# Kernel optimization log

Hardware: AMD Instinct MI355X
Metric: run time of the kernel (lower is better)

Reference implementation:

```python
import jax, jax.numpy as jnp
import numpy as np

# ---- dims ----
B0, CIN, Hh, Ww = 8, 256, 96, 96
SPLIT = 8
DM = CIN // SPLIT            # 32  per-split d_model
EXPAND = 2
DIN = EXPAND * DM            # 64  d_inner
DSTATE = 64
DCONV = 3
HEADDIM = 8
NH = DIN // HEADDIM          # 8 heads
DOUT = 256
CHUNK = 32
D_IN_PROJ = 2 * DIN + 2 * DSTATE + NH  # 264
CONV_CH = DIN + 2 * DSTATE   # 192


def setup_inputs() -> dict:
    key = jax.random.key(0)
    ks = jax.random.split(key, 10)
    x = jax.random.normal(ks[0], (B0, CIN, Hh, Ww), jnp.float32)
    inp = {
        'x': x,
        'ln_w': jnp.ones((CIN,), jnp.float32),
        'ln_b': jnp.zeros((CIN,), jnp.float32),
        'skip_scale': jnp.ones((1,), jnp.float32),
        'proj_w': jax.random.normal(ks[1], (CIN, DOUT), jnp.float32) / np.sqrt(CIN),
        'proj_b': jnp.zeros((DOUT,), jnp.float32),
        'W_in': jax.random.normal(ks[2], (DM, D_IN_PROJ), jnp.float32) / np.sqrt(DM),
        'conv_w': jax.random.normal(ks[3], (CONV_CH, 1, DCONV), jnp.float32) * 0.3,
        'conv_b': jnp.zeros((CONV_CH,), jnp.float32),
        'dt_bias': jax.random.normal(ks[4], (NH,), jnp.float32) * 0.5,
        'A_log': jnp.log(jnp.arange(1.0, NH + 1.0, dtype=jnp.float32)),
        'D': jax.random.normal(ks[5], (NH,), jnp.float32) * 0.5,
        'rms_w': jnp.ones((DIN,), jnp.float32),
        'W_out': jax.random.normal(ks[6], (DIN, DM), jnp.float32) / np.sqrt(DIN),
    }
    return inp


def _layernorm(x, w, b, eps=1e-5):
    mu = jnp.mean(x, -1, keepdims=True)
    xc = x - mu
    var = jnp.mean(xc * xc, -1, keepdims=True)
    return xc * jax.lax.rsqrt(var + eps) * w + b


def _ssd(x, A, Bm, Cm, chunk):
    # x: (b,l,h,p)  A: (b,l,h)  Bm/Cm: (b,l,n); chunked SSD (Mamba2 minimal)
    b, l, h, p = x.shape
    n = Bm.shape[-1]
    nc = l // chunk
    xc = x.reshape(b, nc, chunk, h, p)
    Ac = A.reshape(b, nc, chunk, h).transpose(0, 3, 1, 2)  # (b,h,c,l)
    Bc = Bm.reshape(b, nc, chunk, n)
    Cc = Cm.reshape(b, nc, chunk, n)
    ac = jnp.cumsum(Ac, -1)                                 # (b,h,c,l)
    seg = ac[..., :, None] - ac[..., None, :]
    mask = jnp.tril(jnp.ones((chunk, chunk), bool))
    L = jnp.where(mask, jnp.exp(jnp.where(mask, seg, 0.0)), 0.0)  # (b,h,c,l,s)
    Yd = jnp.einsum('bcln,bcsn,bhcls,bcshp->bclhp', Cc, Bc, L, xc)
    decay_states = jnp.exp(ac[..., -1:] - ac)               # (b,h,c,l)
    states = jnp.einsum('bcln,bhcl,bclhp->bchpn', Bc, decay_states, xc)
    chunk_decay = jnp.exp(ac[..., -1])                      # (b,h,c)
    def step(carry, inp):
        s, d = inp
        return carry * d[..., None, None] + s, carry
    states_t = jnp.moveaxis(states, 1, 0)                   # (c,b,h,p,n)
    dec_t = jnp.moveaxis(chunk_decay, 2, 0)                 # (c,b,h)
    _, prev = jax.lax.scan(step, jnp.zeros_like(states_t[0]), (states_t, dec_t))
    prev = jnp.moveaxis(prev, 0, 1)                         # (b,c,h,p,n)
    Yo = jnp.einsum('bcln,bchpn,bhcl->bclhp', Cc, prev, jnp.exp(ac))
    return (Yd + Yo).reshape(b, l, h, p)


def _mamba2(u, W_in, conv_w, conv_b, dt_bias, A_log, D, rms_w, W_out):
    b, l, _ = u.shape
    zxbcdt = u @ W_in
    z = zxbcdt[..., :DIN]
    xBC = zxbcdt[..., DIN:DIN + CONV_CH]
    dt = jax.nn.softplus(zxbcdt[..., -NH:] + dt_bias)       # (b,l,h)
    conv = jax.lax.conv_general_dilated(
        xBC.transpose(0, 2, 1), conv_w, (1,), [(DCONV - 1, 0)],
        dimension_numbers=('NCH', 'OIH', 'NCH'), feature_group_count=CONV_CH)
    xBC = jax.nn.silu(conv + conv_b[None, :, None]).transpose(0, 2, 1)
    xs = xBC[..., :DIN].reshape(b, l, NH, HEADDIM)
    Bm = xBC[..., DIN:DIN + DSTATE]
    Cm = xBC[..., DIN + DSTATE:]
    A = -jnp.exp(A_log)
    y = _ssd(xs * dt[..., None], dt * A, Bm, Cm, CHUNK)
    y = y + xs * D[None, None, :, None]
    y = y.reshape(b, l, DIN) * jax.nn.silu(z)               # gated
    y = y * jax.lax.rsqrt(jnp.mean(y * y, -1, keepdims=True) + 1e-5) * rms_w
    return y @ W_out


def reference(x, ln_w, ln_b, skip_scale, proj_w, proj_b, W_in, conv_w, conv_b,
              dt_bias, A_log, D, rms_w, W_out):
    Bn, C, h, w = x.shape
    L = h * w
    xf = x.reshape(Bn, C, L).transpose(0, 2, 1)             # (B,L,C)
    xn = _layernorm(xf, ln_w, ln_b)
    d = C // SPLIT
    xs = jnp.moveaxis(xn.reshape(Bn, L, SPLIT, d), 2, 0)    # (S,B,L,d)
    xs = xs.reshape(SPLIT * Bn, L, d)
    ym = _mamba2(xs, W_in, conv_w, conv_b, dt_bias, A_log, D, rms_w, W_out)
    ym = ym + skip_scale * xs
    ym = jnp.moveaxis(ym.reshape(SPLIT, Bn, L, d), 0, 2).reshape(Bn, L, C)
    ym = _layernorm(ym, ln_w, ln_b)
    out = ym @ proj_w + proj_b                              # (B,L,DOUT)
    return out.transpose(0, 2, 1).reshape(Bn, DOUT, h, w)
```

## Files before the change

### kernel.cpp

```cpp
#include <hip/hip_runtime.h>
#include <hip/hip_fp16.h>
#include <math.h>

typedef unsigned short u16;
typedef unsigned int u32;
typedef _Float16 half2_t __attribute__((ext_vector_type(2)));
typedef _Float16 f16x8 __attribute__((ext_vector_type(8)));
typedef float f32x4 __attribute__((ext_vector_type(4)));

#define B0N 8
#define LSEQ 9216
#define NSEQ 64
#define NCHUNK 288
#define DM 32
#define DPROJ 264
#define CONVCH 192
#define XC4 208
#define URH 40
#define CHH 204
#define ZBS 66
#define CH2S 129
#define TTS 40
#define GS 36

#ifndef __has_builtin
#define __has_builtin(x) 0
#endif

__device__ __forceinline__ float silu_(float v) { return v / (1.f + __expf(-v)); }

__global__ __launch_bounds__(256) void k1_ln_split(const float* __restrict__ x,
                                                   const float* __restrict__ lnw,
                                                   const float* __restrict__ lnb,
                                                   __half* __restrict__ u) {
  __shared__ float tile[256 * 33];
  __shared__ float mu[32], rs[32], wv[256], bv[256];
  const int b = blockIdx.y, l0 = blockIdx.x * 32, t = threadIdx.x;
  wv[t] = lnw[t];
  bv[t] = lnb[t];
#pragma unroll 4
  for (int i = 0; i < 32; ++i) {
    int c = i * 8 + (t >> 5), ll = t & 31;
    tile[c * 33 + ll] = x[((size_t)b * 256 + c) * LSEQ + l0 + ll];
  }
  __syncthreads();
  if (t < 32) {
    float s = 0.f, s2 = 0.f;
    for (int c = 0; c < 256; ++c) {
      float v = tile[c * 33 + t];
      s += v; s2 += v * v;
    }
    float m = s * (1.f / 256.f);
    mu[t] = m;
    rs[t] = rsqrtf(s2 * (1.f / 256.f) - m * m + 1e-5f);
  }
  __syncthreads();
#pragma unroll 4
  for (int i = 0; i < 32; ++i) {
    int sp = i >> 2, sub = i & 3;
    int ll = sub * 8 + (t >> 5), dm = t & 31;
    int c = sp * 32 + dm;
    float v = (tile[c * 33 + ll] - mu[ll]) * rs[ll] * wv[c] + bv[c];
    u[(((size_t)(sp * B0N + b)) * LSEQ + l0 + ll) * DM + dm] = __float2half(v);
  }
}

__global__ __launch_bounds__(256, 2) void k2_states(
    const __half* __restrict__ u, const float* __restrict__ Win,
    const float* __restrict__ convw, const float* __restrict__ convb,
    const float* __restrict__ dtbias, const float* __restrict__ Alog,
    __half* __restrict__ S, float* __restrict__ cdec) {
  __shared__ __align__(16) _Float16 ur_h[48 * URH];
  __shared__ __align__(16) float CH2[34 * CH2S];
  __shared__ __align__(16) _Float16 xst[64 * TTS];
  __shared__ __align__(16) _Float16 Bt[64 * TTS];
  __shared__ __align__(16) float dtraw[256], dtv[256], acs[256], wv2[256];
  const int c = blockIdx.x, sq = blockIdx.y, t = threadIdx.x;
  const int l0 = c * 32;
  const int lane = t & 63, wvi = t >> 6, g = lane >> 4, c16 = lane & 15;
  const size_t ubase = (size_t)sq * (LSEQ * DM);
  const f32x4 zero4 = {0.f, 0.f, 0.f, 0.f};

  for (int idx = t; idx < 48 * 32; idx += 256) {
    int r = idx >> 5, dm = idx & 31;
    int l = l0 - 2 + r;
    _Float16 v = (_Float16)0.f;
    if (r < 34 && l >= 0) v = ((const _Float16*)u)[ubase + (size_t)l * DM + dm];
    ur_h[r * URH + dm] = v;
  }
  f16x8 bfr[2];
#pragma unroll
  for (int i = 0; i < 2; ++i) {
    int col = 64 + (wvi + i * 4) * 16 + c16;
#pragma unroll
    for (int j = 0; j < 8; ++j) bfr[i][j] = (_Float16)Win[(g * 8 + j) * DPROJ + col];
  }
  __syncthreads();

  {
    f16x8 am[3];
#pragma unroll
    for (int mt = 0; mt < 3; ++mt)
      am[mt] = *(const f16x8*)&ur_h[(mt * 16 + c16) * URH + g * 8];
#pragma unroll
    for (int i = 0; i < 2; ++i) {
      int colc = (wvi + i * 4) * 16 + c16;
#pragma unroll
      for (int mt = 0; mt < 3; ++mt) {
        f32x4 acc = __builtin_amdgcn_mfma_f32_16x16x32_f16(am[mt], bfr[i], zero4, 0, 0, 0);
#pragma unroll
        for (int r = 0; r < 4; ++r) {
          int R = mt * 16 + 4 * g + r;
          if (R < 34) CH2[R * CH2S + colc] = acc[r];
        }
      }
    }
  }
  __syncthreads();

  {
    const int ch0 = t & 63, lb = t >> 6;
    float cw[2][3], cb[2];
#pragma unroll
    for (int cr = 0; cr < 2; ++cr) {
      int ch = ch0 + cr * 64;
      cw[cr][0] = convw[ch * 3 + 0];
      cw[cr][1] = convw[ch * 3 + 1];
      cw[cr][2] = convw[ch * 3 + 2];
      cb[cr] = convb[ch];
    }
#pragma unroll
    for (int lr = 0; lr < 8; ++lr) {
      int l = lb + lr * 4;
#pragma unroll
      for (int cr = 0; cr < 2; ++cr) {
        int ch = ch0 + cr * 64;
        float v = CH2[l * CH2S + ch] * cw[cr][0] + CH2[(l + 1) * CH2S + ch] * cw[cr][1] +
                  CH2[(l + 2) * CH2S + ch] * cw[cr][2] + cb[cr];
        _Float16 sv = (_Float16)silu_(v);
        if (cr == 0) xst[ch * TTS + l] = sv;
        else Bt[(ch - 64) * TTS + l] = sv;
      }
    }
    int l = t >> 3, h = t & 7;
    float raw = 0.f;
#pragma unroll
    for (int dm = 0; dm < 32; ++dm)
      raw += (float)ur_h[(l + 2) * URH + dm] * Win[dm * DPROJ + 256 + h];
    dtraw[l * 8 + h] = raw;
  }
  __syncthreads();

  {
    const int l = t & 31, h = t >> 5;
    float raw = dtraw[l * 8 + h] + dtbias[h];
    float dt = (raw > 20.f) ? raw : log1pf(__expf(raw));
    float x = dt;
#pragma unroll
    for (int d = 1; d < 32; d <<= 1) {
      float y = __shfl_up(x, d, 32);
      if (l >= d) x += y;
    }
    const float A = -__expf(Alog[h]);
    dtv[t] = dt;
    acs[t] = A * x;
    if (l == 31) cdec[(sq * NCHUNK + c) * 8 + h] = __expf(A * x);
  }
  __syncthreads();

  _Float16* Ah = (_Float16*)CH2;
  {
    int h = t >> 5;
    wv2[t] = __expf(acs[h * 32 + 31] - acs[t]) * dtv[t];
  }
  __syncthreads();
  {
    const int hp = t >> 2, lb2 = (t & 3) * 8;
    const float* w = &wv2[(hp >> 3) * 32 + lb2];
    const _Float16* xr = &xst[hp * TTS + lb2];
    _Float16* ar = &Ah[hp * TTS + lb2];
#pragma unroll
    for (int i = 0; i < 8; ++i) ar[i] = (_Float16)((float)xr[i] * w[i]);
  }
  __syncthreads();

  __half* Sout = (__half*)((char*)CH2 + 5120);
  {
    const int mt = wvi;
    f16x8 aS = *(const f16x8*)&Ah[(mt * 16 + c16) * TTS + g * 8];
#pragma unroll
    for (int nt = 0; nt < 4; ++nt) {
      f16x8 bS = *(const f16x8*)&Bt[(nt * 16 + c16) * TTS + g * 8];
      f32x4 acc = __builtin_amdgcn_mfma_f32_16x16x32_f16(aS, bS, zero4, 0, 0, 0);
#pragma unroll
      for (int r = 0; r < 4; ++r)
        Sout[(mt * 16 + 4 * g + r) * 72 + nt * 16 + c16] = __float2half(acc[r]);
    }
  }
  __syncthreads();
  const size_t sbase = (size_t)(sq * NCHUNK + c) * 4096;
#pragma unroll
  for (int i = 0; i < 2; ++i) {
    int idx = i * 256 + t;
    int hp = idx >> 3, part = idx & 7;
    *(uint4*)(S + sbase + hp * 64 + part * 8) = *(const uint4*)&Sout[hp * 72 + part * 8];
  }
}

__global__ __launch_bounds__(512) void k3_scan(__half* __restrict__ S,
                                               const float* __restrict__ cdec) {
  const int sq = blockIdx.x >> 3, h = blockIdx.x & 7, t = threadIdx.x;
  float carry = 0.f;
  for (int c = 0; c < NCHUNK; ++c) {
    size_t idx = (size_t)(sq * NCHUNK + c) * 4096 + h * 512 + t;
    float s = __half2float(S[idx]);
    S[idx] = __float2half(carry);
    carry = carry * cdec[(sq * NCHUNK + c) * 8 + h] + s;
  }
}

__global__ __launch_bounds__(256, 4) void k4_out(
    const __half* __restrict__ u, const float* __restrict__ Win,
    const float* __restrict__ convw, const float* __restrict__ convb,
    const float* __restrict__ dtbias, const float* __restrict__ Alog,
    const float* __restrict__ Dp, const float* __restrict__ rmsw,
    const float* __restrict__ Wout, const float* __restrict__ skip,
    const __half* __restrict__ S, __half* __restrict__ ym) {
  __shared__ __align__(16) _Float16 ur_h[48 * URH];
  __shared__ __align__(16) _Float16 CHh[34 * CHH];
  __shared__ __align__(16) __half xch[32 * XC4];
  __shared__ __align__(16) float dtraw[256];
  __shared__ __align__(16) float dtv[256], acs[256];
  __shared__ __align__(16) _Float16 zbuf[32 * ZBS];
  const int c = blockIdx.x, sq = blockIdx.y, t = threadIdx.x;
  const int l0 = c * 32;
  const int lane = t & 63, wvi = t >> 6, g = lane >> 4, c16 = lane & 15;
  const size_t ubase = (size_t)sq * (LSEQ * DM);
  const f32x4 zero4 = {0.f, 0.f, 0.f, 0.f};

  const size_t sbase = (size_t)(sq * NCHUNK + c) * 4096;
  uint4 sv0, sv1;
  {
    const uint4* sp = (const uint4*)(S + sbase);
    sv0 = sp[t * 2];
    sv1 = sp[t * 2 + 1];
  }
  for (int idx = t; idx < 48 * 32; idx += 256) {
    int r = idx >> 5, dm = idx & 31;
    int l = l0 - 2 + r;
    _Float16 v = (_Float16)0.f;
    if (r < 34 && l >= 0) v = ((const _Float16*)u)[ubase + (size_t)l * DM + dm];
    ur_h[r * URH + dm] = v;
  }
  f16x8 bfr[3];
#pragma unroll
  for (int i = 0; i < 3; ++i) {
    int col = 64 + (wvi + i * 4) * 16 + c16;
#pragma unroll
    for (int j = 0; j < 8; ++j) bfr[i][j] = (_Float16)Win[(g * 8 + j) * DPROJ + col];
  }
  f16x8 bz;
  {
    int col = wvi * 16 + c16;
#pragma unroll
    for (int j = 0; j < 8; ++j) bz[j] = (_Float16)Win[(g * 8 + j) * DPROJ + col];
  }
  __syncthreads();

  {
    f16x8 am[3];
#pragma unroll
    for (int mt = 0; mt < 3; ++mt)
      am[mt] = *(const f16x8*)&ur_h[(mt * 16 + c16) * URH + g * 8];
#pragma unroll
    for (int i = 0; i < 3; ++i) {
      int colc = (wvi + i * 4) * 16 + c16;
#pragma unroll
      for (int mt = 0; mt < 3; ++mt) {
        f32x4 acc = __builtin_amdgcn_mfma_f32_16x16x32_f16(am[mt], bfr[i], zero4, 0, 0, 0);
#pragma unroll
        for (int r = 0; r < 4; ++r) {
          int R = mt * 16 + 4 * g + r;
          if (R < 34) CHh[R * CHH + colc] = (_Float16)acc[r];
        }
      }
    }
#pragma unroll
    for (int mz = 0; mz < 2; ++mz) {
      f16x8 az = *(const f16x8*)&ur_h[(2 + mz * 16 + c16) * URH + g * 8];
      f32x4 acc = __builtin_amdgcn_mfma_f32_16x16x32_f16(az, bz, zero4, 0, 0, 0);
#pragma unroll
      for (int r = 0; r < 4; ++r) {
        int lY = mz * 16 + 4 * g + r;
        zbuf[lY * ZBS + wvi * 16 + c16] = (_Float16)acc[r];
      }
    }
  }
  __syncthreads();

  {
    const int ch0 = t & 63, lbq = t >> 6;
#pragma unroll
    for (int cr = 0; cr < 3; ++cr) {
      int ch = ch0 + cr * 64;
      float w0 = convw[ch * 3 + 0], w1 = convw[ch * 3 + 1], w2 = convw[ch * 3 + 2];
      float cb = convb[ch];
      float a = (float)CHh[(lbq * 8 + 0) * CHH + ch];
      float b = (float)CHh[(lbq * 8 + 1) * CHH + ch];
#pragma unroll
      for (int j = 0; j < 8; ++j) {
        float cn = (float)CHh[(lbq * 8 + j + 2) * CHH + ch];
        float v = a * w0 + b * w1 + cn * w2 + cb;
        xch[(lbq * 8 + j) * XC4 + ch] = __float2half(silu_(v));
        a = b; b = cn;
      }
    }
    int l = t >> 3, h = t & 7;
    float raw = 0.f;
#pragma unroll
    for (int dm = 0; dm < 32; ++dm)
      raw += (float)ur_h[(l + 2) * URH + dm] * Win[dm * DPROJ + 256 + h];
    dtraw[l * 8 + h] = raw;
  }
  __syncthreads();

  {
    char* pvb = (char*)CHh;
    int hp = t >> 2, part = t & 3;
    *(uint4*)(pvb + hp * 144 + part * 32) = sv0;
    *(uint4*)(pvb + hp * 144 + part * 32 + 16) = sv1;
  }
  {
    const int l = t & 31, h = t >> 5;
    float raw = dtraw[l * 8 + h] + dtbias[h];
    float dt = (raw > 20.f) ? raw : log1pf(__expf(raw));
    float x = dt;
#pragma unroll
    for (int d = 1; d < 32; d <<= 1) {
      float y = __shfl_up(x, d, 32);
      if (l >= d) x += y;
    }
    dtv[t] = dt;
    acs[t] = -__expf(Alog[h]) * x;
  }
  __syncthreads();

  float* Gm = (float*)((char*)CHh + 9216);
  {
    float ev = __expf(acs[t]);
    dtraw[t] = ev;
    const int mt = wvi >> 1, nt = wvi & 1;
    f32x4 acc = zero4;
#pragma unroll
    for (int kk = 0; kk < 2; ++kk) {
      f16x8 aC = *(const f16x8*)&xch[(mt * 16 + c16) * XC4 + 128 + kk * 32 + g * 8];
      f16x8 bB = *(const f16x8*)&xch[(nt * 16 + c16) * XC4 + 64 + kk * 32 + g * 8];
      acc = __builtin_amdgcn_mfma_f32_16x16x32_f16(aC, bB, acc, 0, 0, 0);
    }
#pragma unroll
    for (int r = 0; r < 4; ++r)
      Gm[(mt * 16 + 4 * g + r) * GS + nt * 16 + c16] = acc[r];
  }
  __syncthreads();

  {
    const int s2b = g * 8;
    float gv[2][8];
#pragma unroll
    for (int mt = 0; mt < 2; ++mt) {
      const float* gr = &Gm[(mt * 16 + c16) * GS + s2b];
      float4 g0 = *(const float4*)gr;
      float4 g1 = *(const float4*)(gr + 4);
      gv[mt][0] = g0.x; gv[mt][1] = g0.y; gv[mt][2] = g0.z; gv[mt][3] = g0.w;
      gv[mt][4] = g1.x; gv[mt][5] = g1.y; gv[mt][6] = g1.z; gv[mt][7] = g1.w;
    }
#pragma unroll
    for (int hh = 0; hh < 2; ++hh) {
      const int h = 2 * wvi + hh;
      const float* ap = &acs[h * 32 + s2b];
      const float* dp = &dtv[h * 32 + s2b];
      float4 a0 = *(const float4*)ap, a1 = *(const float4*)(ap + 4);
      float4 d0 = *(const float4*)dp, d1 = *(const float4*)(dp + 4);
      const float av[8] = {a0.x, a0.y, a0.z, a0.w, a1.x, a1.y, a1.z, a1.w};
      const float dv[8] = {d0.x, d0.y, d0.z, d0.w, d1.x, d1.y, d1.z, d1.w};
      f16x8 bfr2;
#pragma unroll
      for (int j = 0; j < 8; ++j)
        bfr2[j] = *(const _Float16*)&xch[(s2b + j) * XC4 + h * 8 + (c16 & 7)];
#pragma unroll
      for (int mt = 0; mt < 2; ++mt) {
        const int row = mt * 16 + c16;
        const float arow = acs[h * 32 + row];
        f16x8 afr;
#pragma unroll
        for (int j = 0; j < 8; ++j) {
          float m = gv[mt][j] * __expf(arow - av[j]) * dv[j];
          afr[j] = (_Float16)((s2b + j <= row) ? m : 0.f);
        }
        f32x4 dacc = __builtin_amdgcn_mfma_f32_16x16x32_f16(afr, bfr2, zero4, 0, 0, 0);
        if (c16 < 8) {
#pragma unroll
          for (int r = 0; r < 4; ++r)
            xch[(mt * 16 + 4 * g + r) * XC4 + 64 + h * 8 + c16] = __float2half(dacc[r]);
        }
      }
    }
  }
  __syncthreads();

  {
    const __half* pvh = (const __half*)CHh;
#pragma unroll
    for (int mt = 0; mt < 2; ++mt) {
      f32x4 acc = zero4;
#pragma unroll
      for (int kk = 0; kk < 2; ++kk) {
        f16x8 aC = *(const f16x8*)&xch[(mt * 16 + c16) * XC4 + 128 + kk * 32 + g * 8];
        f16x8 bP = *(const f16x8*)&pvh[(wvi * 16 + c16) * 72 + kk * 32 + g * 8];
        acc = __builtin_amdgcn_mfma_f32_16x16x32_f16(aC, bP, acc, 0, 0, 0);
      }
      int hp = wvi * 16 + c16;
#pragma unroll
      for (int r = 0; r < 4; ++r) {
        int l = mt * 16 + 4 * g + r;
        float e = dtraw[(hp >> 3) * 32 + l];
        __half* yb = &xch[l * XC4 + 64 + hp];
        *yb = __float2half(__half2float(*yb) + acc[r] * e);
      }
    }
  }
  __syncthreads();

  {
    const int hp = t & 63;
    const float dcoef = Dp[hp >> 3];
#pragma unroll
    for (int k = 0; k < 8; ++k) {
      int l = (k * 256 + t) >> 6;
      float y = __half2float(xch[l * XC4 + 64 + hp]) + (float)xch[l * XC4 + hp] * dcoef;
      float z = (float)zbuf[l * ZBS + hp];
      y *= z / (1.f + __expf(-z));
      xch[l * XC4 + 64 + hp] = __float2half(y);
    }
  }
  __syncthreads();

  float* rp = Gm;
  float* scl = (float*)ur_h;
  {
    const int l = t & 31, seg = t >> 5;
    float p = 0.f;
#pragma unroll
    for (int k = 0; k < 8; ++k) {
      float v = __half2float(xch[l * XC4 + 64 + seg * 8 + k]);
      p += v * v;
    }
    rp[l * 9 + seg] = p;
  }
  __syncthreads();
  if (t < 32) {
    float s2s = 0.f;
#pragma unroll
    for (int seg = 0; seg < 8; ++seg) s2s += rp[t * 9 + seg];
    scl[t] = rsqrtf(s2s * (1.f / 64.f) + 1e-5f);
  }
  __syncthreads();

  for (int idx = t; idx < 2048; idx += 256) {
    int l = idx >> 6, hp = idx & 63;
    xch[l * XC4 + 64 + hp] =
        __float2half(__half2float(xch[l * XC4 + 64 + hp]) * scl[l] * rmsw[hp]);
  }
  __syncthreads();

  {
    const float skipv = skip[0];
    const int mt = wvi >> 1, nt = wvi & 1;
    f32x4 acc = zero4;
#pragma unroll
    for (int kk = 0; kk < 2; ++kk) {
      f16x8 aY = *(const f16x8*)&xch[(mt * 16 + c16) * XC4 + 64 + kk * 32 + g * 8];
      f16x8 bW;
#pragma unroll
      for (int j = 0; j < 8; ++j)
        bW[j] = (_Float16)Wout[(kk * 32 + g * 8 + j) * 32 + nt * 16 + c16];
      acc = __builtin_amdgcn_mfma_f32_16x16x32_f16(aY, bW, acc, 0, 0, 0);
    }
#pragma unroll
    for (int r = 0; r < 4; ++r) {
      int l = mt * 16 + 4 * g + r;
      int dm = nt * 16 + c16;
      size_t gi = ubase + (size_t)(l0 + l) * DM + dm;
      ym[gi] = __float2half(acc[r] + skipv * __half2float(u[gi]));
    }
  }
}

__global__ __launch_bounds__(256) void k5_ln_proj(const __half* __restrict__ ym,
                                                  const float* __restrict__ lnw,
                                                  const float* __restrict__ lnb,
                                                  const float* __restrict__ pw,
                                                  const float* __restrict__ pb,
                                                  float* __restrict__ outp) {
  __shared__ float yf[8448];
  __shared__ float mu[32], rs[32], wv[256], bv[256];
  const int b = blockIdx.y, l0 = blockIdx.x * 32, t = threadIdx.x;
  wv[t] = lnw[t];
  bv[t] = lnb[t];
  for (int sp = 0; sp < 8; ++sp) {
#pragma unroll
    for (int i = 0; i < 4; ++i) {
      int idx = i * 256 + t;
      int ll = idx >> 5, dm = idx & 31;
      yf[ll * 257 + sp * 32 + dm] =
          __half2float(ym[(((size_t)(sp * B0N + b)) * LSEQ + l0 + ll) * DM + dm]);
    }
  }
  __syncthreads();
  if (t < 32) {
    float s = 0.f, s2 = 0.f;
    for (int ch = 0; ch < 256; ++ch) {
      float v = yf[t * 257 + ch];
      s += v; s2 += v * v;
    }
    float m = s * (1.f / 256.f);
    mu[t] = m;
    rs[t] = rsqrtf(s2 * (1.f / 256.f) - m * m + 1e-5f);
  }
  __syncthreads();
#pragma unroll 8
  for (int i = 0; i < 32; ++i) {
    int idx = i * 256 + t;
    int ll = idx >> 8, ch = idx & 255;
    yf[ll * 257 + ch] = (yf[ll * 257 + ch] - mu[ll]) * rs[ll] * wv[ch] + bv[ch];
  }
  __syncthreads();
  const int llg = t >> 5, og = t & 31;
  float acc[4][8];
#pragma unroll
  for (int k = 0; k < 4; ++k)
#pragma unroll
    for (int j = 0; j < 8; ++j) acc[k][j] = 0.f;
  for (int ch = 0; ch < 256; ++ch) {
    const float4 w0 = *(const float4*)(pw + (size_t)ch * 256 + og * 8);
    const float4 w1 = *(const float4*)(pw + (size_t)ch * 256 + og * 8 + 4);
#pragma unroll
    for (int k = 0; k < 4; ++k) {
      float y = yf[(llg * 4 + k) * 257 + ch];
      acc[k][0] += y * w0.x; acc[k][1] += y * w0.y; acc[k][2] += y * w0.z; acc[k][3] += y * w0.w;
      acc[k][4] += y * w1.x; acc[k][5] += y * w1.y; acc[k][6] += y * w1.z; acc[k][7] += y * w1.w;
    }
  }
  __syncthreads();
  float* res = yf;
#pragma unroll
  for (int j = 0; j < 8; ++j) {
    float bias = pb[og * 8 + j];
#pragma unroll
    for (int k = 0; k < 4; ++k)
      res[(og * 8 + j) * 33 + llg * 4 + k] = acc[k][j] + bias;
  }
  __syncthreads();
  for (int idx = t; idx < 8192; idx += 256) {
    int o = idx >> 5, l = idx & 31;
    outp[((size_t)(b * 256 + o)) * LSEQ + l0 + l] = res[o * 33 + l];
  }
}

extern "C" void kernel_launch(void* const* d_in, const int* in_sizes, int n_in,
                              void* d_out, int out_size, void* d_ws, size_t ws_size,
                              hipStream_t stream) {
  (void)in_sizes; (void)n_in; (void)out_size;
  const float* x     = (const float*)d_in[0];
  const float* lnw   = (const float*)d_in[1];
  const float* lnb   = (const float*)d_in[2];
  const float* skip  = (const float*)d_in[3];
  const float* pw    = (const float*)d_in[4];
  const float* pb    = (const float*)d_in[5];
  const float* Win   = (const float*)d_in[6];
  const float* convw = (const float*)d_in[7];
  const float* convb = (const float*)d_in[8];
  const float* dtb   = (const float*)d_in[9];
  const float* Alog  = (const float*)d_in[10];
  const float* Dp    = (const float*)d_in[11];
  const float* rmsw  = (const float*)d_in[12];
  const float* Wout  = (const float*)d_in[13];
  float* outp = (float*)d_out;

  const size_t NEED = 227082240ull;
  if (ws_size < NEED) return;
  char* ws = (char*)d_ws;
  __half* u    = (__half*)ws;
  __half* S    = (__half*)(ws + 37748736);
  float*  cdec = (float*)(ws + 188743680);
  __half* ym   = (__half*)(ws + 189333504);

  k1_ln_split<<<dim3(288, 8), 256, 0, stream>>>(x, lnw, lnb, u);
  k2_states<<<dim3(288, 64), 256, 0, stream>>>(u, Win, convw, convb, dtb, Alog, S, cdec);
  k3_scan<<<dim3(512), 512, 0, stream>>>(S, cdec);
  k4_out<<<dim3(288, 64), 256, 0, stream>>>(u, Win, convw, convb, dtb, Alog, Dp, rmsw,
                                            Wout, skip, S, ym);
  k5_ln_proj<<<dim3(288, 8), 256, 0, stream>>>(ym, lnw, lnb, pw, pb, outp);
}
```

Measured before the change: 722.0 us.

## Use fp16 MFMA for final projection and parallelize LayerNorm reductions

Rewrites the final LayerNorm+projection kernel to stage activations as fp16 in shared memory and compute the 256x256 projection with MFMA 16x16x32 f16 instructions instead of scalar FP32 FMAs. Both LayerNorm kernels now spread the per-token mean/variance reduction over all 256 threads with partial sums instead of 32 threads walking 256 channels serially. It also raises the occupancy hint. The cost is lower precision in the normalized activations and weights (fp16) and per-element scalar weight loads converted to half.

```diff
diff --git a/kernel.cpp b/kernel.cpp
--- a/kernel.cpp
+++ b/kernel.cpp
@@ -22,6 +22,7 @@
 #define CH2S 129
 #define TTS 40
 #define GS 36
+#define YH5 264
 
 #ifndef __has_builtin
 #define __has_builtin(x) 0
@@ -35,6 +36,7 @@
                                                    __half* __restrict__ u) {
   __shared__ float tile[256 * 33];
   __shared__ float mu[32], rs[32], wv[256], bv[256];
+  __shared__ float ps[32 * 9], ps2[32 * 9];
   const int b = blockIdx.y, l0 = blockIdx.x * 32, t = threadIdx.x;
   wv[t] = lnw[t];
   bv[t] = lnb[t];
@@ -44,12 +46,22 @@
     tile[c * 33 + ll] = x[((size_t)b * 256 + c) * LSEQ + l0 + ll];
   }
   __syncthreads();
+  {
+    const int ll = t & 31, seg = t >> 5;
+    float s = 0.f, s2 = 0.f;
+#pragma unroll 8
+    for (int i = 0; i < 32; ++i) {
+      float v = tile[(seg * 32 + i) * 33 + ll];
+      s += v; s2 += v * v;
+    }
+    ps[ll * 9 + seg] = s;
+    ps2[ll * 9 + seg] = s2;
+  }
+  __syncthreads();
   if (t < 32) {
     float s = 0.f, s2 = 0.f;
-    for (int c = 0; c < 256; ++c) {
-      float v = tile[c * 33 + t];
-      s += v; s2 += v * v;
-    }
+#pragma unroll
+    for (int seg = 0; seg < 8; ++seg) { s += ps[t * 9 + seg]; s2 += ps2[t * 9 + seg]; }
     float m = s * (1.f / 256.f);
     mu[t] = m;
     rs[t] = rsqrtf(s2 * (1.f / 256.f) - m * m + 1e-5f);
@@ -496,69 +508,87 @@
   }
 }
 
-__global__ __launch_bounds__(256) void k5_ln_proj(const __half* __restrict__ ym,
-                                                  const float* __restrict__ lnw,
-                                                  const float* __restrict__ lnb,
-                                                  const float* __restrict__ pw,
-                                                  const float* __restrict__ pb,
-                                                  float* __restrict__ outp) {
-  __shared__ float yf[8448];
+__global__ __launch_bounds__(256, 4) void k5_ln_proj(const __half* __restrict__ ym,
+                                                     const float* __restrict__ lnw,
+                                                     const float* __restrict__ lnb,
+                                                     const float* __restrict__ pw,
+                                                     const float* __restrict__ pb,
+                                                     float* __restrict__ outp) {
+  __shared__ __align__(16) char buf[33792];
   __shared__ float mu[32], rs[32], wv[256], bv[256];
+  __shared__ float ps[32 * 9], ps2[32 * 9];
+  _Float16* yh = (_Float16*)buf;
+  float* res = (float*)buf;
   const int b = blockIdx.y, l0 = blockIdx.x * 32, t = threadIdx.x;
+  const int lane = t & 63, wvi = t >> 6, g = lane >> 4, c16 = lane & 15;
+  const f32x4 zero4 = {0.f, 0.f, 0.f, 0.f};
   wv[t] = lnw[t];
   bv[t] = lnb[t];
   for (int sp = 0; sp < 8; ++sp) {
 #pragma unroll
-    for (int i = 0; i < 4; ++i) {
+    for (int i = 0; i < 2; ++i) {
       int idx = i * 256 + t;
-      int ll = idx >> 5, dm = idx & 31;
-      yf[ll * 257 + sp * 32 + dm] =
-          __half2float(ym[(((size_t)(sp * B0N + b)) * LSEQ + l0 + ll) * DM + dm]);
-    }
+      int ll = idx >> 4, dmp = (idx & 15) * 2;
+      u32 v = *(const u32*)&ym[(((size_t)(sp * B0N + b)) * LSEQ + l0 + ll) * DM + dmp];
+      *(u32*)&yh[ll * YH5 + sp * 32 + dmp] = v;
+    }
+  }
+  __syncthreads();
+  {
+    const int ll = t & 31, seg = t >> 5;
+    float s = 0.f, s2 = 0.f;
+#pragma unroll 8
+    for (int i = 0; i < 32; ++i) {
+      float v = (float)yh[ll * YH5 + seg * 32 + i];
+      s += v; s2 += v * v;
+    }
+    ps[ll * 9 + seg] = s;
+    ps2[ll * 9 + seg] = s2;
   }
   __syncthreads();
   if (t < 32) {
     float s = 0.f, s2 = 0.f;
-    for (int ch = 0; ch < 256; ++ch) {
-      float v = yf[t * 257 + ch];
-      s += v; s2 += v * v;
-    }
+#pragma unroll
+    for (int seg = 0; seg < 8; ++seg) { s += ps[t * 9 + seg]; s2 += ps2[t * 9 + seg]; }
     float m = s * (1.f / 256.f);
     mu[t] = m;
     rs[t] = rsqrtf(s2 * (1.f / 256.f) - m * m + 1e-5f);
   }
   __syncthreads();
-#pragma unroll 8
+#pragma unroll
   for (int i = 0; i < 32; ++i) {
     int idx = i * 256 + t;
     int ll = idx >> 8, ch = idx & 255;
-    yf[ll * 257 + ch] = (yf[ll * 257 + ch] - mu[ll]) * rs[ll] * wv[ch] + bv[ch];
-  }
-  __syncthreads();
-  const int llg = t >> 5, og = t & 31;
-  float acc[4][8];
-#pragma unroll
-  for (int k = 0; k < 4; ++k)
-#pragma unroll
-    for (int j = 0; j < 8; ++j) acc[k][j] = 0.f;
-  for (int ch = 0; ch < 256; ++ch) {
-    const float4 w0 = *(const float4*)(pw + (size_t)ch * 256 + og * 8);
-    const float4 w1 = *(const float4*)(pw + (size_t)ch * 256 + og * 8 + 4);
-#pragma unroll
-    for (int k = 0; k < 4; ++k) {
-      float y = yf[(llg * 4 + k) * 257 + ch];
-      acc[k][0] += y * w0.x; acc[k][1] += y * w0.y; acc[k][2] += y * w0.z; acc[k][3] += y * w0.w;
-      acc[k][4] += y * w1.x; acc[k][5] += y * w1.y; acc[k][6] += y * w1.z; acc[k][7] += y * w1.w;
-    }
-  }
-  __syncthreads();
-  float* res = yf;
-#pragma unroll
-  for (int j = 0; j < 8; ++j) {
-    float bias = pb[og * 8 + j];
-#pragma unroll
-    for (int k = 0; k < 4; ++k)
-      res[(og * 8 + j) * 33 + llg * 4 + k] = acc[k][j] + bias;
+    float v = ((float)yh[ll * YH5 + ch] - mu[ll]) * rs[ll] * wv[ch] + bv[ch];
+    yh[ll * YH5 + ch] = (_Float16)v;
+  }
+  __syncthreads();
+  f16x8 am[16];
+#pragma unroll
+  for (int mt = 0; mt < 2; ++mt)
+#pragma unroll
+    for (int kk = 0; kk < 8; ++kk)
+      am[mt * 8 + kk] = *(const f16x8*)&yh[(mt * 16 + c16) * YH5 + kk * 32 + g * 8];
+  __syncthreads();
+#pragma unroll
+  for (int ni = 0; ni < 4; ++ni) {
+    const int col = (wvi + ni * 4) * 16 + c16;
+    f32x4 acc0 = zero4, acc1 = zero4;
+#pragma unroll
+    for (int kk = 0; kk < 8; ++kk) {
+      f16x8 bW;
+#pragma unroll
+      for (int j = 0; j < 8; ++j)
+        bW[j] = (_Float16)pw[(size_t)(kk * 32 + g * 8 + j) * 256 + col];
+      acc0 = __builtin_amdgcn_mfma_f32_16x16x32_f16(am[kk], bW, acc0, 0, 0, 0);
+      acc1 = __builtin_amdgcn_mfma_f32_16x16x32_f16(am[8 + kk], bW, acc1, 0, 0, 0);
+    }
+    const float bias = pb[col];
+#pragma unroll
+    for (int r = 0; r < 4; ++r) {
+      res[col * 33 + 4 * g + r] = acc0[r] + bias;
+      res[col * 33 + 16 + 4 * g + r] = acc1[r] + bias;
+    }
   }
   __syncthreads();
   for (int idx = t; idx < 8192; idx += 256) {
```

Measured after the change: 636.5 us. 1.13x faster.
